# Kernel tuning notes

Measured on AMD Instinct MI355X. Metric: run time of the kernel, lower is better.

The kernel has to match this reference:

```python
import jax, jax.numpy as jnp
import numpy as np

K = 7      # kernel size per spatial dim (kernel=[7,7])
PAD = 3    # padding per side ('same' for stride 1)
COUT = 64  # output width of the per-patch linear func


def _unfold(x):
    """convPrep: pad + unfold into sliding-window patches.
    x: [B, H, W] -> patches [B, H, W, K*K] (im2col, zero 'constant' padding)."""
    p = jax.lax.conv_general_dilated_patches(
        x[:, None, :, :],                # [B, 1, H, W]
        filter_shape=(K, K),
        window_strides=(1, 1),
        padding=[(PAD, PAD), (PAD, PAD)])
    # p: [B, K*K, H, W] -> [B, H, W, K*K]
    return jnp.moveaxis(p, 1, -1)


def setup_inputs() -> dict:
    key = jax.random.key(0)
    k1, k2 = jax.random.split(key, 2)
    x = jax.random.normal(k1, (8, 384, 384), dtype=jnp.float32)
    W = jax.random.normal(k2, (K * K, COUT), dtype=jnp.float32) / np.sqrt(K * K).astype(np.float32)
    b = jnp.zeros((COUT,), dtype=jnp.float32)
    return {"x": x, "W": W, "b": b}


def reference(x, W, b):
    # convPrep (pad+unfold) -> func (linear per flattened patch) -> convPost (fold back)
    patches = _unfold(x)                               # [B, H, W, K*K]
    out = jnp.einsum('bhwk,kc->bhwc', patches, W) + b  # [B, H, W, COUT]
    return out
```

## Files before the change

### kernel.cpp

```cpp
#include <hip/hip_runtime.h>


#define HH 384
#define WW 384
#define BB 8
#define CC 64
#define TPW 16
#define TROW (WW / TPW)
#define NTILES (BB * HH * TROW)
#define NBLOCKS 2048
#define WPB 4
#define NWAVES (NBLOCKS * WPB)
#define TPWAVE (NTILES / NWAVES)

typedef __attribute__((ext_vector_type(8))) __bf16 bf16x8;
typedef __attribute__((ext_vector_type(4))) float f32x4;

__global__ __launch_bounds__(256)
void conv7_mfma_nt(const float* __restrict__ xg, const float* __restrict__ wg,
                   const float* __restrict__ bg, float* __restrict__ out)
{
    const int tid  = threadIdx.x;
    const int lane = tid & 63;
    const int wv   = tid >> 6;
    const int lq   = lane >> 4;
    const int lr   = lane & 15;

    bf16x8 wfr[2][4];
#pragma unroll
    for (int ch = 0; ch < 2; ++ch)
#pragma unroll
        for (int g = 0; g < 4; ++g) {
            bf16x8 f;
#pragma unroll
            for (int j = 0; j < 8; ++j) {
                const int ky = ch * 4 + lq;
                const int kx = j;
                f[j] = (ky < 7 && kx < 7) ? (__bf16)wg[(ky * 7 + kx) * CC + g * 16 + lr]
                                          : (__bf16)0.f;
            }
            wfr[ch][g] = f;
        }
    f32x4 biasf[4];
#pragma unroll
    for (int g = 0; g < 4; ++g)
        biasf[g] = *(const f32x4*)(bg + g * 16 + lq * 4);

    const int gw = blockIdx.x * WPB + wv;

    for (int it = 0; it < TPWAVE; ++it) {
        const int tile = gw * TPWAVE + it;
        const int tw = tile % TROW;
        const int rh = tile / TROW;
        const int h  = rh % HH;
        const int b  = rh / HH;
        const int w0 = tw * TPW;

        bf16x8 xf[2];
        const bool interior = (h >= 3) & (h <= HH - 5) & (w0 != 0) & (w0 != WW - TPW);
        if (interior) {
            const float* p0 = xg + ((size_t)b * HH + (h - 3)) * WW + (w0 - 3 + lr);
#pragma unroll
            for (int ch = 0; ch < 2; ++ch) {
                float v[8];
                __builtin_memcpy(v, p0 + (size_t)(ch * 4 + lq) * WW, 32);
                bf16x8 f;
#pragma unroll
                for (int j = 0; j < 8; ++j) f[j] = (__bf16)v[j];
                xf[ch] = f;
            }
        } else {
#pragma unroll
            for (int ch = 0; ch < 2; ++ch) {
                const int r  = h - 3 + ch * 4 + lq;
                const int rc = r < 0 ? 0 : (r > HH - 1 ? HH - 1 : r);
                const bool rok = (r >= 0) & (r < HH);
                const float* prow = xg + ((size_t)b * HH + rc) * WW;
                bf16x8 f;
#pragma unroll
                for (int j = 0; j < 8; ++j) {
                    const int c  = w0 - 3 + lr + j;
                    const int cc = c < 0 ? 0 : (c > WW - 1 ? WW - 1 : c);
                    float v = prow[cc];
                    v = (rok & (c >= 0) & (c < WW)) ? v : 0.f;
                    f[j] = (__bf16)v;
                }
                xf[ch] = f;
            }
        }

        f32x4 acc[4];
#pragma unroll
        for (int g = 0; g < 4; ++g) acc[g] = biasf[g];
#pragma unroll
        for (int ch = 0; ch < 2; ++ch)
#pragma unroll
            for (int g = 0; g < 4; ++g)
                acc[g] = __builtin_amdgcn_mfma_f32_16x16x32_bf16(
                    wfr[ch][g], xf[ch], acc[g], 0, 0, 0);

        float* op = out + (((size_t)b * HH + h) * WW + w0 + lr) * CC + lq * 4;
#pragma unroll
        for (int g = 0; g < 4; ++g)
            __builtin_nontemporal_store(acc[g], (f32x4*)(op + g * 16));
    }
}

extern "C" void kernel_launch(void* const* d_in, const int* in_sizes, int n_in,
                              void* d_out, int out_size, void* d_ws, size_t ws_size,
                              hipStream_t stream) {
    const float* x = (const float*)d_in[0];
    const float* w = (const float*)d_in[1];
    const float* b = (const float*)d_in[2];
    float* out = (float*)d_out;
    (void)in_sizes; (void)n_in; (void)out_size; (void)d_ws; (void)ws_size;
    conv7_mfma_nt<<<NBLOCKS, 256, 0, stream>>>(x, w, b, out);
}
```

Measured before the change: 343.4 us.

## Split channels across wave pairs and coalesce output stores via LDS transpose

Each tile is now computed by a pair of waves, each producing 32 of the 64 output channels, with 512-thread blocks. Accumulators are staged through shared memory so each store instruction writes contiguous 128-byte row segments instead of scattered 16-byte pieces, and the bias is added after the transpose. The goal is better write coalescing on an output-bandwidth-bound kernel and more waves in flight. In exchange, both waves of a pair load the same input patch, and the code adds LDS round trips and drops the nontemporal store hint.

```diff
diff --git a/kernel.cpp b/kernel.cpp
--- a/kernel.cpp
+++ b/kernel.cpp
@@ -9,47 +9,49 @@
 #define TROW (WW / TPW)
 #define NTILES (BB * HH * TROW)
 #define NBLOCKS 2048
-#define WPB 4
-#define NWAVES (NBLOCKS * WPB)
-#define TPWAVE (NTILES / NWAVES)
+#define PPB 4
+#define NPAIRS (NBLOCKS * PPB)
+#define TPPAIR (NTILES / NPAIRS)
 
 typedef __attribute__((ext_vector_type(8))) __bf16 bf16x8;
 typedef __attribute__((ext_vector_type(4))) float f32x4;
 
-__global__ __launch_bounds__(256)
-void conv7_mfma_nt(const float* __restrict__ xg, const float* __restrict__ wg,
+__global__ __launch_bounds__(512)
+void conv7_mfma_w8(const float* __restrict__ xg, const float* __restrict__ wg,
                    const float* __restrict__ bg, float* __restrict__ out)
 {
+    __shared__ float lt[8][16][36];
+
     const int tid  = threadIdx.x;
     const int lane = tid & 63;
     const int wv   = tid >> 6;
     const int lq   = lane >> 4;
     const int lr   = lane & 15;
+    const int pr   = wv >> 1;
+    const int cb   = (wv & 1) * 32;
 
-    bf16x8 wfr[2][4];
+    bf16x8 wfr[2][2];
 #pragma unroll
     for (int ch = 0; ch < 2; ++ch)
 #pragma unroll
-        for (int g = 0; g < 4; ++g) {
+        for (int g = 0; g < 2; ++g) {
             bf16x8 f;
 #pragma unroll
             for (int j = 0; j < 8; ++j) {
                 const int ky = ch * 4 + lq;
                 const int kx = j;
-                f[j] = (ky < 7 && kx < 7) ? (__bf16)wg[(ky * 7 + kx) * CC + g * 16 + lr]
-                                          : (__bf16)0.f;
+                f[j] = (ky < 7 && kx < 7)
+                     ? (__bf16)wg[(ky * 7 + kx) * CC + cb + g * 16 + lr]
+                     : (__bf16)0.f;
             }
             wfr[ch][g] = f;
         }
-    f32x4 biasf[4];
-#pragma unroll
-    for (int g = 0; g < 4; ++g)
-        biasf[g] = *(const f32x4*)(bg + g * 16 + lq * 4);
+    const f32x4 biast = *(const f32x4*)(bg + cb + (lane & 7) * 4);
 
-    const int gw = blockIdx.x * WPB + wv;
+    const int gp = blockIdx.x * PPB + pr;
 
-    for (int it = 0; it < TPWAVE; ++it) {
-        const int tile = gw * TPWAVE + it;
+    for (int it = 0; it < TPPAIR; ++it) {
+        const int tile = gp * TPPAIR + it;
         const int tw = tile % TROW;
         const int rh = tile / TROW;
         const int h  = rh % HH;
@@ -89,20 +91,28 @@
             }
         }
 
-        f32x4 acc[4];
-#pragma unroll
-        for (int g = 0; g < 4; ++g) acc[g] = biasf[g];
+        f32x4 acc[2] = {(f32x4){0.f,0.f,0.f,0.f}, (f32x4){0.f,0.f,0.f,0.f}};
 #pragma unroll
         for (int ch = 0; ch < 2; ++ch)
 #pragma unroll
-            for (int g = 0; g < 4; ++g)
+            for (int g = 0; g < 2; ++g)
                 acc[g] = __builtin_amdgcn_mfma_f32_16x16x32_bf16(
                     wfr[ch][g], xf[ch], acc[g], 0, 0, 0);
 
-        float* op = out + (((size_t)b * HH + h) * WW + w0 + lr) * CC + lq * 4;
+        float* lw = &lt[wv][lr][0];
 #pragma unroll
-        for (int g = 0; g < 4; ++g)
-            __builtin_nontemporal_store(acc[g], (f32x4*)(op + g * 16));
+        for (int g = 0; g < 2; ++g)
+            *(f32x4*)(lw + g * 16 + lq * 4) = acc[g];
+        f32x4 ov[2];
+#pragma unroll
+        for (int g = 0; g < 2; ++g) {
+            ov[g] = *(const f32x4*)(&lt[wv][g * 8 + (lane >> 3)][(lane & 7) * 4]);
+            ov[g] += biast;
+        }
+        float* op = out + (((size_t)b * HH + h) * WW + w0) * CC + cb;
+#pragma unroll
+        for (int g = 0; g < 2; ++g)
+            *(f32x4*)(op + (size_t)(g * 8 + (lane >> 3)) * CC + (lane & 7) * 4) = ov[g];
     }
 }
 
@@ -114,5 +124,5 @@
     const float* b = (const float*)d_in[2];
     float* out = (float*)d_out;
     (void)in_sizes; (void)n_in; (void)out_size; (void)d_ws; (void)ws_size;
-    conv7_mfma_nt<<<NBLOCKS, 256, 0, stream>>>(x, w, b, out);
+    conv7_mfma_w8<<<NBLOCKS, 512, 0, stream>>>(x, w, b, out);
 }
```

After: 316.2 us. 1.09x faster.
